# Kernel tuning notes

Measured on AMD Instinct MI355X. Metric: run time of the kernel, lower is better.

The kernel has to match this reference:

```python
import jax, jax.numpy as jnp
import numpy as np

N, E, B = 3000, 96000, 64
CIN, MID = 8, 16
G1, G2 = 32, 8
FC1, FC2, OUT = 512, 128, 10
EPS = 1e-5


def setup_inputs() -> dict:
    key = jax.random.key(0)
    ks = jax.random.split(key, 40)
    u = lambda k, shape, s: jax.random.uniform(k, shape, jnp.float32, -s, s)
    inp = {}
    inp['x'] = jax.random.normal(ks[0], (N, B, CIN), jnp.float32)
    inp['edge_index'] = jax.random.randint(ks[1], (2, E), 0, N, jnp.int64)
    # SAGEConv params (uniform(-1/sqrt(in_channels), ...))
    s = 1.0 / np.sqrt(CIN)
    inp['edge_w_raw'] = jnp.ones((E,), jnp.float32) * 0.01
    inp['sage_self_w'] = u(ks[2], (CIN, MID), s)
    inp['sage_w'] = u(ks[3], (CIN, MID), s)
    inp['sage_b'] = u(ks[4], (MID,), s)
    # LayerNorm over (num_nodes, mid_channel)
    inp['ln_g'] = jnp.ones((N, MID), jnp.float32)
    inp['ln_b'] = jnp.zeros((N, MID), jnp.float32)
    # 1x1 Conv2d stacks (stored as [out,in] matrices) + BatchNorm2d (eval stats)
    inp['conv1_w'] = jax.random.normal(ks[5], (G1, MID), jnp.float32) * np.sqrt(2.0 / G1)
    inp['conv1_b'] = u(ks[6], (G1,), 1.0 / np.sqrt(MID))
    inp['bn1_g'] = jax.random.uniform(ks[7], (G1,), jnp.float32, 0.5, 1.5)
    inp['bn1_b'] = jax.random.normal(ks[8], (G1,), jnp.float32) * 0.1
    inp['bn1_m'] = jax.random.normal(ks[9], (G1,), jnp.float32) * 0.1
    inp['bn1_v'] = jax.random.uniform(ks[10], (G1,), jnp.float32, 0.5, 1.5)
    inp['conv2_w'] = jax.random.normal(ks[11], (G2, G1), jnp.float32) * np.sqrt(2.0 / G2)
    inp['conv2_b'] = u(ks[12], (G2,), 1.0 / np.sqrt(G1))
    inp['bn2_g'] = jax.random.uniform(ks[13], (G2,), jnp.float32, 0.5, 1.5)
    inp['bn2_b'] = jax.random.normal(ks[14], (G2,), jnp.float32) * 0.1
    inp['bn2_m'] = jax.random.normal(ks[15], (G2,), jnp.float32) * 0.1
    inp['bn2_v'] = jax.random.uniform(ks[16], (G2,), jnp.float32, 0.5, 1.5)
    # FC stack: Linear(G2*N, FC1) + BN1d, Linear(FC1, FC2) + BN1d, fc1
    d0 = G2 * N
    inp['fc_w1'] = jax.random.normal(ks[17], (FC1, d0), jnp.float32) * np.sqrt(2.0 / (d0 + FC1))
    inp['fc_b1'] = jnp.full((FC1,), 0.01, jnp.float32)
    inp['bnf1_g'] = jax.random.uniform(ks[18], (FC1,), jnp.float32, 0.5, 1.5)
    inp['bnf1_b'] = jax.random.normal(ks[19], (FC1,), jnp.float32) * 0.1
    inp['bnf1_m'] = jax.random.normal(ks[20], (FC1,), jnp.float32) * 0.1
    inp['bnf1_v'] = jax.random.uniform(ks[21], (FC1,), jnp.float32, 0.5, 1.5)
    inp['fc_w2'] = jax.random.normal(ks[22], (FC2, FC1), jnp.float32) * np.sqrt(2.0 / (FC1 + FC2))
    inp['fc_b2'] = jnp.full((FC2,), 0.01, jnp.float32)
    inp['bnf2_g'] = jax.random.uniform(ks[23], (FC2,), jnp.float32, 0.5, 1.5)
    inp['bnf2_b'] = jax.random.normal(ks[24], (FC2,), jnp.float32) * 0.1
    inp['bnf2_m'] = jax.random.normal(ks[25], (FC2,), jnp.float32) * 0.1
    inp['bnf2_v'] = jax.random.uniform(ks[26], (FC2,), jnp.float32, 0.5, 1.5)
    inp['fc1_w'] = jax.random.normal(ks[27], (OUT, FC2), jnp.float32) * np.sqrt(2.0 / (FC2 + OUT))
    inp['fc1_b'] = jnp.full((OUT,), 0.01, jnp.float32)
    return inp


def _bn(y, g, b, m, v):
    # eval-mode BatchNorm; y is [B, C, N] or [B, C]
    if y.ndim == 3:
        return (y - m[:, None]) * (g[:, None] / jnp.sqrt(v[:, None] + EPS)) + b[:, None]
    return (y - m) * (g / jnp.sqrt(v + EPS)) + b


def reference(x, edge_index, edge_w_raw, sage_self_w, sage_w, sage_b, ln_g, ln_b,
              conv1_w, conv1_b, bn1_g, bn1_b, bn1_m, bn1_v,
              conv2_w, conv2_b, bn2_g, bn2_b, bn2_m, bn2_v,
              fc_w1, fc_b1, bnf1_g, bnf1_b, bnf1_m, bnf1_v,
              fc_w2, fc_b2, bnf2_g, bnf2_b, bnf2_m, bnf2_v,
              fc1_w, fc1_b):
    row, col = edge_index[0], edge_index[1]
    ew = jax.nn.sigmoid(edge_w_raw)
    # SAGEConv: gather -> weighted message -> scatter-mean by col -> matmul
    msg = x[row] * ew[:, None, None]                          # [E, B, CIN]
    summed = jax.ops.segment_sum(msg, col, num_segments=N)    # [N, B, CIN]
    cnt = jax.ops.segment_sum(jnp.ones((E,), x.dtype), col, num_segments=N)
    agg = summed / jnp.maximum(cnt, 1.0)[:, None, None]
    neigh = jnp.einsum('nbc,cm->nbm', agg, sage_w) + sage_b   # [N, B, MID]
    self_out = jnp.einsum('nbc,cm->nbm', x, sage_self_w)
    h = 0.0 * self_out + 1.0 * neigh                          # alphas = [0, 1]
    h = jax.nn.relu(h)
    # LayerNorm over (num_nodes, mid) per batch element
    hb = jnp.transpose(h, (1, 0, 2))                          # [B, N, MID]
    mu = hb.mean(axis=(1, 2), keepdims=True)
    var = hb.var(axis=(1, 2), keepdims=True)
    hb = (hb - mu) / jnp.sqrt(var + EPS) * ln_g + ln_b
    y = jnp.transpose(hb, (0, 2, 1))                          # [B, MID, N]
    # 1x1 conv stack (relu then BN, matching source order)
    y = jnp.einsum('om,bmn->bon', conv1_w, y) + conv1_b[:, None]
    y = _bn(jax.nn.relu(y), bn1_g, bn1_b, bn1_m, bn1_v)
    y = jnp.einsum('oc,bcn->bon', conv2_w, y) + conv2_b[:, None]
    y = _bn(jax.nn.relu(y), bn2_g, bn2_b, bn2_m, bn2_v)       # [B, G2, N]
    z = y.reshape(y.shape[0], -1)                             # [B, G2*N]
    z = jax.nn.relu(_bn(z @ fc_w1.T + fc_b1, bnf1_g, bnf1_b, bnf1_m, bnf1_v))
    z = jax.nn.relu(_bn(z @ fc_w2.T + fc_b2, bnf2_g, bnf2_b, bnf2_m, bnf2_v))
    logits = z @ fc1_w.T + fc1_b
    return jax.nn.softmax(logits, axis=-1), logits
```

## Files before the change

### kernel.cpp

```cpp
#include <hip/hip_runtime.h>
#include <hip/hip_bf16.h>
#include <math.h>

#define NN   3000
#define EE   96000
#define BB   64
#define CIN  8
#define MID  16
#define G1   32
#define G2   8
#define FC1N 512
#define FC2N 128
#define OUTN 10
#define EPSV 1e-5f

#define BC   (BB * CIN)
#define HROW (NN * MID)
#define D0   (G2 * NN)

#define P_EWRAW 0
#define P_SW    96000
#define P_SB    96128
#define P_LNG   96144
#define P_LNB   144144
#define P_C1W   192144
#define P_C1B   192656
#define P_BN1G  192688
#define P_BN1B  192720
#define P_BN1M  192752
#define P_BN1V  192784
#define P_C2W   192816
#define P_C2B   193072
#define P_BN2G  193080
#define P_BN2B  193088
#define P_BN2M  193096
#define P_BN2V  193104
#define P_FB1   193112
#define P_BF1G  193624
#define P_BF1B  194136
#define P_BF1M  194648
#define P_BF1V  195160
#define P_FW2   195672
#define P_FB2   261208
#define P_BF2G  261336
#define P_BF2B  261464
#define P_BF2M  261592
#define P_BF2V  261720
#define P_FOW   261848
#define P_FOB   263128
#define P_TOT   263138

#define KCH  320
#define NKC  75

__device__ __forceinline__ float b2f(unsigned short u) {
    union { unsigned int i; float f; } c;
    c.i = ((unsigned int)u) << 16;
    return c.f;
}

__device__ __forceinline__ unsigned short f2b_rne(float x) {
    union { float f; unsigned int u; } c; c.f = x;
    unsigned int r = c.u + 0x7FFFu + ((c.u >> 16) & 1u);
    return (unsigned short)(r >> 16);
}

typedef __attribute__((ext_vector_type(8))) short short8;
typedef __attribute__((ext_vector_type(4))) float f32x4;

struct PTab { const void* p[30]; };
__global__ __launch_bounds__(256)
void k_prep(const void* __restrict__ ei_raw, const unsigned int* __restrict__ ewr,
            PTab tab,
            int* __restrict__ ei32, int* __restrict__ cnt, int* __restrict__ flags,
            float* __restrict__ P) {
    __shared__ int sh_is64, sh_bf;
    if (threadIdx.x == 0) {
        const int* pw = (const int*)ei_raw;
        int any = 0;
        #pragma unroll
        for (int i = 1; i < 32; i += 2) any |= pw[i];
        sh_is64 = (any == 0) ? 1 : 0;
        unsigned int w = ewr[0];
        sh_bf = ((w >> 16) == (w & 0xFFFFu)) ? 1 : 0;
        if (blockIdx.x == 0) flags[0] = sh_bf;
    }
    __syncthreads();
    int bf = sh_bf;
    long long gi = (long long)blockIdx.x * blockDim.x + threadIdx.x;
    if (gi < 2 * EE) {
        int i = (int)gi;
        int v = sh_is64 ? (int)((const long long*)ei_raw)[i]
                        : ((const int*)ei_raw)[i];
        ei32[i] = v;
        if (i >= EE) atomicAdd(&cnt[v], 1);
        return;
    }
    gi -= 2 * EE;
    if (gi >= P_TOT) return;
    int i = (int)gi;
    const int off[31] = {
        P_EWRAW, P_SW, P_SB, P_LNG, P_LNB, P_C1W, P_C1B, P_BN1G, P_BN1B, P_BN1M,
        P_BN1V, P_C2W, P_C2B, P_BN2G, P_BN2B, P_BN2M, P_BN2V, P_FB1, P_BF1G,
        P_BF1B, P_BF1M, P_BF1V, P_FW2, P_FB2, P_BF2G, P_BF2B, P_BF2M, P_BF2V,
        P_FOW, P_FOB, P_TOT };
    int r = 0;
    #pragma unroll
    for (int j = 1; j < 31; ++j) r += (i >= off[j]) ? 1 : 0;
    int e = i - off[r];
    P[i] = bf ? b2f(((const unsigned short*)tab.p[r])[e])
              : ((const float*)tab.p[r])[e];
}

__global__ void k_scan(const int* __restrict__ cnt, int* __restrict__ off,
                       int* __restrict__ cursor) {
    __shared__ int part[1024];
    int t = threadIdx.x;
    int base = t * 3;
    int c0 = 0, c1 = 0, c2 = 0;
    if (base     < NN) c0 = cnt[base];
    if (base + 1 < NN) c1 = cnt[base + 1];
    if (base + 2 < NN) c2 = cnt[base + 2];
    int s = c0 + c1 + c2;
    part[t] = s;
    __syncthreads();
    for (int d = 1; d < 1024; d <<= 1) {
        int v = (t >= d) ? part[t - d] : 0;
        __syncthreads();
        part[t] += v;
        __syncthreads();
    }
    int excl = part[t] - s;
    if (base < NN)     { off[base]     = excl;           cursor[base]     = excl; }
    if (base + 1 < NN) { off[base + 1] = excl + c0;      cursor[base + 1] = excl + c0; }
    if (base + 2 < NN) { off[base + 2] = excl + c0 + c1; cursor[base + 2] = excl + c0 + c1; }
    if (t == 1023) off[NN] = part[1023];
}

__global__ void k_scatter(const int* __restrict__ ei, const float* __restrict__ ew,
                          int* __restrict__ cursor,
                          int* __restrict__ rcsr, float* __restrict__ wcsr) {
    int e = blockIdx.x * blockDim.x + threadIdx.x;
    if (e < EE) {
        int p = atomicAdd(&cursor[ei[EE + e]], 1);
        rcsr[p] = ei[e];
        wcsr[p] = 1.f / (1.f + expf(-ew[e]));
    }
}

__global__ __launch_bounds__(256)
void k_agg_sage(const void* __restrict__ xraw, const int* __restrict__ flags,
                const int* __restrict__ off,
                const int* __restrict__ rcsr, const float* __restrict__ wcsr,
                const float* __restrict__ sw, const float* __restrict__ sb,
                float* __restrict__ hb) {
    __shared__ float aggL[BC];
    __shared__ float swL[CIN * MID];
    __shared__ float sbL[MID];
    int n = blockIdx.x;
    int t = threadIdx.x;
    if (t < CIN * MID) swL[t] = sw[t];
    if (t < MID)       sbL[t] = sb[t];
    int k0 = off[n], k1 = off[n + 1];
    float a0 = 0.f, a1 = 0.f, b0 = 0.f, b1 = 0.f;
    int k = k0;
    if (flags[0]) {
        const unsigned int* xu = (const unsigned int*)xraw;
        for (; k + 3 < k1; k += 4) {
            int   r0 = rcsr[k],     r1 = rcsr[k + 1];
            int   r2 = rcsr[k + 2], r3 = rcsr[k + 3];
            float w0 = wcsr[k],     w1 = wcsr[k + 1];
            float w2 = wcsr[k + 2], w3 = wcsr[k + 3];
            unsigned int u0 = xu[(size_t)r0 * 256 + t];
            unsigned int u1 = xu[(size_t)r1 * 256 + t];
            unsigned int u2 = xu[(size_t)r2 * 256 + t];
            unsigned int u3 = xu[(size_t)r3 * 256 + t];
            a0 += b2f((unsigned short)(u0 & 0xFFFFu)) * w0;
            a1 += b2f((unsigned short)(u0 >> 16))     * w0;
            b0 += b2f((unsigned short)(u1 & 0xFFFFu)) * w1;
            b1 += b2f((unsigned short)(u1 >> 16))     * w1;
            a0 += b2f((unsigned short)(u2 & 0xFFFFu)) * w2;
            a1 += b2f((unsigned short)(u2 >> 16))     * w2;
            b0 += b2f((unsigned short)(u3 & 0xFFFFu)) * w3;
            b1 += b2f((unsigned short)(u3 >> 16))     * w3;
        }
        for (; k < k1; ++k) {
            int r0 = rcsr[k];
            float w0 = wcsr[k];
            unsigned int u0 = xu[(size_t)r0 * 256 + t];
            a0 += b2f((unsigned short)(u0 & 0xFFFFu)) * w0;
            a1 += b2f((unsigned short)(u0 >> 16))     * w0;
        }
        float inv = 1.f / fmaxf((float)(k1 - k0), 1.f);
        aggL[2 * t]     = (a0 + b0) * inv;
        aggL[2 * t + 1] = (a1 + b1) * inv;
    } else {
        const float* x = (const float*)xraw;
        for (; k + 3 < k1; k += 4) {
            int   r0 = rcsr[k],     r1 = rcsr[k + 1];
            int   r2 = rcsr[k + 2], r3 = rcsr[k + 3];
            float w0 = wcsr[k],     w1 = wcsr[k + 1];
            float w2 = wcsr[k + 2], w3 = wcsr[k + 3];
            const float* xp0 = x + (size_t)r0 * BC;
            const float* xp1 = x + (size_t)r1 * BC;
            const float* xp2 = x + (size_t)r2 * BC;
            const float* xp3 = x + (size_t)r3 * BC;
            a0 += xp0[t]       * w0;  a1 += xp0[t + 256] * w0;
            b0 += xp1[t]       * w1;  b1 += xp1[t + 256] * w1;
            a0 += xp2[t]       * w2;  a1 += xp2[t + 256] * w2;
            b0 += xp3[t]       * w3;  b1 += xp3[t + 256] * w3;
        }
        for (; k < k1; ++k) {
            int r0 = rcsr[k];
            float w0 = wcsr[k];
            const float* xp0 = x + (size_t)r0 * BC;
            a0 += xp0[t] * w0;
            a1 += xp0[t + 256] * w0;
        }
        float inv = 1.f / fmaxf((float)(k1 - k0), 1.f);
        aggL[t]       = (a0 + b0) * inv;
        aggL[t + 256] = (a1 + b1) * inv;
    }
    __syncthreads();
    #pragma unroll
    for (int r4 = 0; r4 < 4; ++r4) {
        int q = t + r4 * 256;
        int b = q >> 4, m = q & 15;
        float v = sbL[m];
        const float* ag = &aggL[b * CIN];
        #pragma unroll
        for (int c = 0; c < CIN; ++c) v += ag[c] * swL[c * MID + m];
        v = fmaxf(v, 0.f);
        hb[(size_t)b * HROW + n * MID + m] = v;
    }
}

__global__ __launch_bounds__(256)
void k_ln_stats(const float* __restrict__ hb, float* __restrict__ stats) {
    __shared__ float ssum[256], ssq[256];
    int b = blockIdx.x, t = threadIdx.x;
    const float4* p = (const float4*)(hb + (size_t)b * HROW);
    float s = 0.f, q = 0.f;
    for (int i = t; i < HROW / 4; i += 256) {
        float4 v = p[i];
        s += v.x + v.y + v.z + v.w;
        q += v.x * v.x + v.y * v.y + v.z * v.z + v.w * v.w;
    }
    ssum[t] = s; ssq[t] = q;
    __syncthreads();
    for (int d = 128; d > 0; d >>= 1) {
        if (t < d) { ssum[t] += ssum[t + d]; ssq[t] += ssq[t + d]; }
        __syncthreads();
    }
    if (t == 0) {
        float mu = ssum[0] / (float)HROW;
        float var = ssq[0] / (float)HROW - mu * mu;
        stats[b]      = mu;
        stats[BB + b] = 1.f / sqrtf(var + EPSV);
    }
}

__global__ __launch_bounds__(256)
void k_conv_stack(const float* __restrict__ hb, const float* __restrict__ stats,
                  const float* __restrict__ P, unsigned short* __restrict__ zT) {
    __shared__ float hbt[64 * 65];
    __shared__ float w1s[G1 * MID], w2s[G2 * G1];
    __shared__ float c1s[G1], s1[G1], t1[G1];
    __shared__ float c2s[G2], s2[G2], t2[G2];
    int t = threadIdx.x;
    int n0 = blockIdx.x * 4;
    for (int j = t; j < G1 * MID; j += 256) w1s[j] = P[P_C1W + j];
    if (t < G2 * G1)  w2s[t] = P[P_C2W + t];
    if (t < G1) {
        float s = P[P_BN1G + t] / sqrtf(P[P_BN1V + t] + EPSV);
        c1s[t] = P[P_C1B + t]; s1[t] = s; t1[t] = P[P_BN1B + t] - P[P_BN1M + t] * s;
    }
    if (t < G2) {
        float s = P[P_BN2G + t] / sqrtf(P[P_BN2V + t] + EPSV);
        c2s[t] = P[P_C2B + t]; s2[t] = s; t2[t] = P[P_BN2B + t] - P[P_BN2M + t] * s;
    }
    #pragma unroll
    for (int r = 0; r < 4; ++r) {
        int i = r * 256 + t;
        int b = i >> 4, q = i & 15;
        float4 v = *(const float4*)(hb + (size_t)b * HROW + n0 * MID + q * 4);
        int ld = b * 65 + q * 4;
        hbt[ld] = v.x; hbt[ld + 1] = v.y; hbt[ld + 2] = v.z; hbt[ld + 3] = v.w;
    }
    __syncthreads();
    int nl = t >> 6, b = t & 63;
    int n = n0 + nl;
    float mu = stats[b], rs = stats[BB + b];
    float tv[MID];
    #pragma unroll
    for (int m = 0; m < MID; ++m) {
        float g = P[P_LNG + n * MID + m], lb = P[P_LNB + n * MID + m];
        tv[m] = (hbt[b * 65 + nl * MID + m] - mu) * rs * g + lb;
    }
    float v1[G1];
    #pragma unroll
    for (int o = 0; o < G1; ++o) {
        float d = c1s[o];
        #pragma unroll
        for (int m = 0; m < MID; ++m) d += w1s[o * MID + m] * tv[m];
        d = fmaxf(d, 0.f);
        v1[o] = d * s1[o] + t1[o];
    }
    #pragma unroll
    for (int o2 = 0; o2 < G2; ++o2) {
        float d = c2s[o2];
        #pragma unroll
        for (int c = 0; c < G1; ++c) d += w2s[o2 * G1 + c] * v1[c];
        d = fmaxf(d, 0.f);
        zT[((size_t)(o2 * NN + n)) * BB + b] = f2b_rne(d * s2[o2] + t2[o2]);
    }
}

__global__ __launch_bounds__(256)
void k_fc1(const unsigned short* __restrict__ zT, const void* __restrict__ w1raw,
           const int* __restrict__ flags, float* __restrict__ out1p) {
    __shared__ unsigned int zs[64 * 20];
    int kc = blockIdx.y;
    int t = threadIdx.x;
    int lane = t & 63;
    int wv = t >> 6;
    int n = lane & 15;
    int q = lane >> 4;
    int fbase = blockIdx.x * 64 + wv * 16;
    int bf = flags[0];
    const size_t kcb = (size_t)kc * KCH;
    const float*          w1f = (const float*)w1raw;
    const unsigned short* w1b = (const unsigned short*)w1raw;

    f32x4 acc0 = {0.f, 0.f, 0.f, 0.f};
    f32x4 acc1 = {0.f, 0.f, 0.f, 0.f};
    f32x4 acc2 = {0.f, 0.f, 0.f, 0.f};
    f32x4 acc3 = {0.f, 0.f, 0.f, 0.f};

    int zb = t & 63;
    int kg = t >> 6;

    for (int ks = 0; ks < KCH / 32; ++ks) {
        size_t k0 = kcb + (size_t)ks * 32;
        const unsigned short* zsrc = zT + (k0 + kg * 8) * BB + zb;
        unsigned short zv[8];
        #pragma unroll
        for (int j = 0; j < 8; ++j) zv[j] = zsrc[j * BB];
        unsigned int pk0 = (unsigned int)zv[0] | ((unsigned int)zv[1] << 16);
        unsigned int pk1 = (unsigned int)zv[2] | ((unsigned int)zv[3] << 16);
        unsigned int pk2 = (unsigned int)zv[4] | ((unsigned int)zv[5] << 16);
        unsigned int pk3 = (unsigned int)zv[6] | ((unsigned int)zv[7] << 16);
        __syncthreads();
        *(uint4*)&zs[zb * 20 + kg * 4] = make_uint4(pk0, pk1, pk2, pk3);
        short8 av;
        if (bf) {
            av = *(const short8*)(w1b + (size_t)(fbase + n) * D0 + k0 + q * 8);
        } else {
            const float* wr = w1f + (size_t)(fbase + n) * D0 + k0 + q * 8;
            float4 wa = *(const float4*)wr;
            float4 wb = *(const float4*)(wr + 4);
            av[0] = (short)f2b_rne(wa.x); av[1] = (short)f2b_rne(wa.y);
            av[2] = (short)f2b_rne(wa.z); av[3] = (short)f2b_rne(wa.w);
            av[4] = (short)f2b_rne(wb.x); av[5] = (short)f2b_rne(wb.y);
            av[6] = (short)f2b_rne(wb.z); av[7] = (short)f2b_rne(wb.w);
        }
        __syncthreads();
        const char* zbase = (const char*)zs + q * 16;
        short8 bv0 = *(const short8*)(zbase + (0  + n) * 80);
        short8 bv1 = *(const short8*)(zbase + (16 + n) * 80);
        short8 bv2 = *(const short8*)(zbase + (32 + n) * 80);
        short8 bv3 = *(const short8*)(zbase + (48 + n) * 80);
        acc0 = __builtin_amdgcn_mfma_f32_16x16x32_bf16(av, bv0, acc0, 0, 0, 0);
        acc1 = __builtin_amdgcn_mfma_f32_16x16x32_bf16(av, bv1, acc1, 0, 0, 0);
        acc2 = __builtin_amdgcn_mfma_f32_16x16x32_bf16(av, bv2, acc2, 0, 0, 0);
        acc3 = __builtin_amdgcn_mfma_f32_16x16x32_bf16(av, bv3, acc3, 0, 0, 0);
    }
    float* op = out1p + ((size_t)kc * FC1N + fbase + q * 4) * BB + n;
    #pragma unroll
    for (int r = 0; r < 4; ++r) {
        op[r * BB +  0] = acc0[r];
        op[r * BB + 16] = acc1[r];
        op[r * BB + 32] = acc2[r];
        op[r * BB + 48] = acc3[r];
    }
}

__global__ void k_fc1_fin(const float* __restrict__ out1p, const float* __restrict__ P,
                          float* __restrict__ z1) {
    int i = blockIdx.x * blockDim.x + threadIdx.x;
    if (i < BB * FC1N) {
        int f = i >> 6, b = i & 63;
        float acc = 0.f;
        for (int kc = 0; kc < NKC; ++kc)
            acc += out1p[((size_t)kc * FC1N + f) * BB + b];
        acc += P[P_FB1 + f];
        float s = P[P_BF1G + f] / sqrtf(P[P_BF1V + f] + EPSV);
        acc = (acc - P[P_BF1M + f]) * s + P[P_BF1B + f];
        z1[b * FC1N + f] = fmaxf(acc, 0.f);
    }
}

__global__ __launch_bounds__(128)
void k_fc2head(const float* __restrict__ z1, const float* __restrict__ P,
               const int* __restrict__ flags, void* __restrict__ outv) {
    __shared__ float zsrc[FC1N];
    __shared__ float z2s[FC2N];
    __shared__ float lg[OUTN];
    __shared__ float red[2];
    int b = blockIdx.x, t = threadIdx.x;
    #pragma unroll
    for (int r = 0; r < 4; ++r) zsrc[t + r * 128] = z1[b * FC1N + t + r * 128];
    __syncthreads();
    {
        int f = t;
        const float4* wr = (const float4*)(P + P_FW2 + (size_t)f * FC1N);
        const float4* zr = (const float4*)zsrc;
        float acc = P[P_FB2 + f];
        for (int k = 0; k < FC1N / 4; ++k) {
            float4 wv = wr[k];
            float4 zv = zr[k];
            acc += wv.x * zv.x + wv.y * zv.y + wv.z * zv.z + wv.w * zv.w;
        }
        float s = P[P_BF2G + f] / sqrtf(P[P_BF2V + f] + EPSV);
        acc = (acc - P[P_BF2M + f]) * s + P[P_BF2B + f];
        z2s[f] = fmaxf(acc, 0.f);
    }
    __syncthreads();
    if (t < OUTN) {
        float acc = P[P_FOB + t];
        const float* wr = P + P_FOW + t * FC2N;
        for (int k = 0; k < FC2N; ++k) acc += wr[k] * z2s[k];
        lg[t] = acc;
    }
    __syncthreads();
    if (t == 0) {
        float mx = lg[0];
        for (int o = 1; o < OUTN; ++o) mx = fmaxf(mx, lg[o]);
        float s = 0.f;
        for (int o = 0; o < OUTN; ++o) s += expf(lg[o] - mx);
        red[0] = mx; red[1] = s;
    }
    __syncthreads();
    if (t < OUTN) {
        float p = expf(lg[t] - red[0]) / red[1];
        if (flags[0]) {
            __hip_bfloat16* o = (__hip_bfloat16*)outv;
            o[b * OUTN + t] = __float2bfloat16(p);
            o[BB * OUTN + b * OUTN + t] = __float2bfloat16(lg[t]);
        } else {
            float* o = (float*)outv;
            o[b * OUTN + t] = p;
            o[BB * OUTN + b * OUTN + t] = lg[t];
        }
    }
}

extern "C" void kernel_launch(void* const* d_in, const int* in_sizes, int n_in,
                              void* d_out, int out_size, void* d_ws, size_t ws_size,
                              hipStream_t stream) {
    char* ws = (char*)d_ws;
    size_t o = 0;
    auto carve = [&](size_t bytes) { void* p = ws + o; o += (bytes + 255) & ~(size_t)255; return p; };
    int*   flags  = (int*)  carve(16);
    int*   ei32   = (int*)  carve((size_t)2 * EE * sizeof(int));
    int*   cnt    = (int*)  carve(NN * sizeof(int));
    int*   off    = (int*)  carve((NN + 1) * sizeof(int));
    int*   cursor = (int*)  carve(NN * sizeof(int));
    int*   rcsr   = (int*)  carve(EE * sizeof(int));
    float* wcsr   = (float*)carve(EE * sizeof(float));
    float* P      = (float*)carve((size_t)P_TOT * sizeof(float));
    float* hb     = (float*)carve((size_t)BB * HROW * sizeof(float));
    float* stats  = (float*)carve(2 * BB * sizeof(float));
    unsigned short* zT = (unsigned short*)carve((size_t)D0 * BB * sizeof(unsigned short));
    float* out1p  = (float*)carve((size_t)NKC * FC1N * BB * sizeof(float));
    float* z1     = (float*)carve(BB * FC1N * sizeof(float));

    hipMemsetAsync(cnt, 0, NN * sizeof(int), stream);

    PTab tab;
    tab.p[0]  = d_in[2];   tab.p[1]  = d_in[4];   tab.p[2]  = d_in[5];
    tab.p[3]  = d_in[6];   tab.p[4]  = d_in[7];   tab.p[5]  = d_in[8];
    tab.p[6]  = d_in[9];   tab.p[7]  = d_in[10];  tab.p[8]  = d_in[11];
    tab.p[9]  = d_in[12];  tab.p[10] = d_in[13];  tab.p[11] = d_in[14];
    tab.p[12] = d_in[15];  tab.p[13] = d_in[16];  tab.p[14] = d_in[17];
    tab.p[15] = d_in[18];  tab.p[16] = d_in[19];  tab.p[17] = d_in[21];
    tab.p[18] = d_in[22];  tab.p[19] = d_in[23];  tab.p[20] = d_in[24];
    tab.p[21] = d_in[25];  tab.p[22] = d_in[26];  tab.p[23] = d_in[27];
    tab.p[24] = d_in[28];  tab.p[25] = d_in[29];  tab.p[26] = d_in[30];
    tab.p[27] = d_in[31];  tab.p[28] = d_in[32];  tab.p[29] = d_in[33];

    long long prep_tot = 2LL * EE + P_TOT;
    k_prep<<<(int)((prep_tot + 255) / 256), 256, 0, stream>>>(
        d_in[1], (const unsigned int*)d_in[2], tab, ei32, cnt, flags, P);

    k_scan   <<<1, 1024, 0, stream>>>(cnt, off, cursor);
    k_scatter<<<(EE + 255) / 256, 256, 0, stream>>>(ei32, P + P_EWRAW, cursor, rcsr, wcsr);
    k_agg_sage<<<NN, 256, 0, stream>>>(d_in[0], flags, off, rcsr, wcsr,
                                       P + P_SW, P + P_SB, hb);
    k_ln_stats<<<BB, 256, 0, stream>>>(hb, stats);
    k_conv_stack<<<NN / 4, 256, 0, stream>>>(hb, stats, P, zT);
    dim3 g7(FC1N / 64, NKC);
    k_fc1    <<<g7, 256, 0, stream>>>(zT, d_in[20], flags, out1p);
    k_fc1_fin<<<(BB * FC1N + 255) / 256, 256, 0, stream>>>(out1p, P, z1);
    k_fc2head<<<BB, 128, 0, stream>>>(z1, P, flags, (void*)d_out);
}
```

Before: 259.8 us.

## Fuse all stages into one persistent cooperative kernel with grid syncs

Replaces the chain of nine separate kernel launches plus a memset with a single cooperative persistent kernel. Stages are separated by grid-wide barriers, and each stage loops over its work with grid-stride indexing. LayerNorm statistics appear to be gathered during aggregation, and the FC1 K dimension is padded and rechunked to 64 chunks of 384. The aim is to remove launch gaps and extra passes. The costs are a grid capped at 512 blocks, occupancy limited to 2 blocks per SM, and serial phases such as the single-block scan that leave most of the GPU idle.

```diff
diff --git a/kernel.cpp b/kernel.cpp
--- a/kernel.cpp
+++ b/kernel.cpp
@@ -1,6 +1,9 @@
 #include <hip/hip_runtime.h>
 #include <hip/hip_bf16.h>
+#include <hip/hip_cooperative_groups.h>
 #include <math.h>
+
+namespace cg = cooperative_groups;
 
 #define NN   3000
 #define EE   96000
@@ -50,15 +53,15 @@
 #define P_FOB   263128
 #define P_TOT   263138
 
-#define KCH  320
-#define NKC  75
+#define KPAD 24576
+#define KCH  384
+#define NKC  64
 
 __device__ __forceinline__ float b2f(unsigned short u) {
     union { unsigned int i; float f; } c;
     c.i = ((unsigned int)u) << 16;
     return c.f;
 }
-
 __device__ __forceinline__ unsigned short f2b_rne(float x) {
     union { float f; unsigned int u; } c; c.f = x;
     unsigned int r = c.u + 0x7FFFu + ((c.u >> 16) & 1u);
@@ -69,388 +72,406 @@
 typedef __attribute__((ext_vector_type(4))) float f32x4;
 
 struct PTab { const void* p[30]; };
-__global__ __launch_bounds__(256)
-void k_prep(const void* __restrict__ ei_raw, const unsigned int* __restrict__ ewr,
-            PTab tab,
-            int* __restrict__ ei32, int* __restrict__ cnt, int* __restrict__ flags,
-            float* __restrict__ P) {
-    __shared__ int sh_is64, sh_bf;
-    if (threadIdx.x == 0) {
-        const int* pw = (const int*)ei_raw;
+
+struct MegaArgs {
+    const void* ei_raw;
+    const void* x_raw;
+    const void* w1raw;
+    PTab tab;
+    int* ei32; int* cnt; int* offA; int* cursor;
+    int* rcsr; float* wcsr; float* P;
+    float* hb; float* statsS; float* statsQ;
+    unsigned short* zT;
+    float* out1p; float* z1;
+    void* outv;
+};
+
+__global__ __launch_bounds__(256, 2)
+void k_mega(MegaArgs A) {
+    cg::grid_group grid = cg::this_grid();
+    __shared__ __align__(16) char smem[20768];
+    __shared__ int sh2[2];
+    const int t  = threadIdx.x;
+    const int nb = gridDim.x;
+    const int bid = blockIdx.x;
+
+    if (t == 0) {
+        const int* pw = (const int*)A.ei_raw;
         int any = 0;
         #pragma unroll
         for (int i = 1; i < 32; i += 2) any |= pw[i];
-        sh_is64 = (any == 0) ? 1 : 0;
-        unsigned int w = ewr[0];
-        sh_bf = ((w >> 16) == (w & 0xFFFFu)) ? 1 : 0;
-        if (blockIdx.x == 0) flags[0] = sh_bf;
+        sh2[0] = (any == 0) ? 1 : 0;
+        unsigned int w = ((const unsigned int*)A.tab.p[0])[0];
+        sh2[1] = ((w >> 16) == (w & 0xFFFFu)) ? 1 : 0;
     }
     __syncthreads();
-    int bf = sh_bf;
-    long long gi = (long long)blockIdx.x * blockDim.x + threadIdx.x;
-    if (gi < 2 * EE) {
-        int i = (int)gi;
-        int v = sh_is64 ? (int)((const long long*)ei_raw)[i]
-                        : ((const int*)ei_raw)[i];
-        ei32[i] = v;
-        if (i >= EE) atomicAdd(&cnt[v], 1);
-        return;
-    }
-    gi -= 2 * EE;
-    if (gi >= P_TOT) return;
-    int i = (int)gi;
-    const int off[31] = {
-        P_EWRAW, P_SW, P_SB, P_LNG, P_LNB, P_C1W, P_C1B, P_BN1G, P_BN1B, P_BN1M,
-        P_BN1V, P_C2W, P_C2B, P_BN2G, P_BN2B, P_BN2M, P_BN2V, P_FB1, P_BF1G,
-        P_BF1B, P_BF1M, P_BF1V, P_FW2, P_FB2, P_BF2G, P_BF2B, P_BF2M, P_BF2V,
-        P_FOW, P_FOB, P_TOT };
-    int r = 0;
-    #pragma unroll
-    for (int j = 1; j < 31; ++j) r += (i >= off[j]) ? 1 : 0;
-    int e = i - off[r];
-    P[i] = bf ? b2f(((const unsigned short*)tab.p[r])[e])
-              : ((const float*)tab.p[r])[e];
-}
-
-__global__ void k_scan(const int* __restrict__ cnt, int* __restrict__ off,
-                       int* __restrict__ cursor) {
-    __shared__ int part[1024];
-    int t = threadIdx.x;
-    int base = t * 3;
-    int c0 = 0, c1 = 0, c2 = 0;
-    if (base     < NN) c0 = cnt[base];
-    if (base + 1 < NN) c1 = cnt[base + 1];
-    if (base + 2 < NN) c2 = cnt[base + 2];
-    int s = c0 + c1 + c2;
-    part[t] = s;
-    __syncthreads();
-    for (int d = 1; d < 1024; d <<= 1) {
-        int v = (t >= d) ? part[t - d] : 0;
-        __syncthreads();
-        part[t] += v;
-        __syncthreads();
-    }
-    int excl = part[t] - s;
-    if (base < NN)     { off[base]     = excl;           cursor[base]     = excl; }
-    if (base + 1 < NN) { off[base + 1] = excl + c0;      cursor[base + 1] = excl + c0; }
-    if (base + 2 < NN) { off[base + 2] = excl + c0 + c1; cursor[base + 2] = excl + c0 + c1; }
-    if (t == 1023) off[NN] = part[1023];
-}
-
-__global__ void k_scatter(const int* __restrict__ ei, const float* __restrict__ ew,
-                          int* __restrict__ cursor,
-                          int* __restrict__ rcsr, float* __restrict__ wcsr) {
-    int e = blockIdx.x * blockDim.x + threadIdx.x;
-    if (e < EE) {
-        int p = atomicAdd(&cursor[ei[EE + e]], 1);
-        rcsr[p] = ei[e];
-        wcsr[p] = 1.f / (1.f + expf(-ew[e]));
-    }
-}
-
-__global__ __launch_bounds__(256)
-void k_agg_sage(const void* __restrict__ xraw, const int* __restrict__ flags,
-                const int* __restrict__ off,
-                const int* __restrict__ rcsr, const float* __restrict__ wcsr,
-                const float* __restrict__ sw, const float* __restrict__ sb,
-                float* __restrict__ hb) {
-    __shared__ float aggL[BC];
-    __shared__ float swL[CIN * MID];
-    __shared__ float sbL[MID];
-    int n = blockIdx.x;
-    int t = threadIdx.x;
-    if (t < CIN * MID) swL[t] = sw[t];
-    if (t < MID)       sbL[t] = sb[t];
-    int k0 = off[n], k1 = off[n + 1];
-    float a0 = 0.f, a1 = 0.f, b0 = 0.f, b1 = 0.f;
-    int k = k0;
-    if (flags[0]) {
-        const unsigned int* xu = (const unsigned int*)xraw;
-        for (; k + 3 < k1; k += 4) {
-            int   r0 = rcsr[k],     r1 = rcsr[k + 1];
-            int   r2 = rcsr[k + 2], r3 = rcsr[k + 3];
-            float w0 = wcsr[k],     w1 = wcsr[k + 1];
-            float w2 = wcsr[k + 2], w3 = wcsr[k + 3];
-            unsigned int u0 = xu[(size_t)r0 * 256 + t];
-            unsigned int u1 = xu[(size_t)r1 * 256 + t];
-            unsigned int u2 = xu[(size_t)r2 * 256 + t];
-            unsigned int u3 = xu[(size_t)r3 * 256 + t];
-            a0 += b2f((unsigned short)(u0 & 0xFFFFu)) * w0;
-            a1 += b2f((unsigned short)(u0 >> 16))     * w0;
-            b0 += b2f((unsigned short)(u1 & 0xFFFFu)) * w1;
-            b1 += b2f((unsigned short)(u1 >> 16))     * w1;
-            a0 += b2f((unsigned short)(u2 & 0xFFFFu)) * w2;
-            a1 += b2f((unsigned short)(u2 >> 16))     * w2;
-            b0 += b2f((unsigned short)(u3 & 0xFFFFu)) * w3;
-            b1 += b2f((unsigned short)(u3 >> 16))     * w3;
-        }
-        for (; k < k1; ++k) {
-            int r0 = rcsr[k];
-            float w0 = wcsr[k];
-            unsigned int u0 = xu[(size_t)r0 * 256 + t];
-            a0 += b2f((unsigned short)(u0 & 0xFFFFu)) * w0;
-            a1 += b2f((unsigned short)(u0 >> 16))     * w0;
-        }
-        float inv = 1.f / fmaxf((float)(k1 - k0), 1.f);
-        aggL[2 * t]     = (a0 + b0) * inv;
-        aggL[2 * t + 1] = (a1 + b1) * inv;
-    } else {
-        const float* x = (const float*)xraw;
-        for (; k + 3 < k1; k += 4) {
-            int   r0 = rcsr[k],     r1 = rcsr[k + 1];
-            int   r2 = rcsr[k + 2], r3 = rcsr[k + 3];
-            float w0 = wcsr[k],     w1 = wcsr[k + 1];
-            float w2 = wcsr[k + 2], w3 = wcsr[k + 3];
-            const float* xp0 = x + (size_t)r0 * BC;
-            const float* xp1 = x + (size_t)r1 * BC;
-            const float* xp2 = x + (size_t)r2 * BC;
-            const float* xp3 = x + (size_t)r3 * BC;
-            a0 += xp0[t]       * w0;  a1 += xp0[t + 256] * w0;
-            b0 += xp1[t]       * w1;  b1 += xp1[t + 256] * w1;
-            a0 += xp2[t]       * w2;  a1 += xp2[t + 256] * w2;
-            b0 += xp3[t]       * w3;  b1 += xp3[t + 256] * w3;
-        }
-        for (; k < k1; ++k) {
-            int r0 = rcsr[k];
-            float w0 = wcsr[k];
-            const float* xp0 = x + (size_t)r0 * BC;
-            a0 += xp0[t] * w0;
-            a1 += xp0[t + 256] * w0;
-        }
-        float inv = 1.f / fmaxf((float)(k1 - k0), 1.f);
-        aggL[t]       = (a0 + b0) * inv;
-        aggL[t + 256] = (a1 + b1) * inv;
-    }
-    __syncthreads();
-    #pragma unroll
-    for (int r4 = 0; r4 < 4; ++r4) {
-        int q = t + r4 * 256;
-        int b = q >> 4, m = q & 15;
-        float v = sbL[m];
-        const float* ag = &aggL[b * CIN];
+    const int is64 = sh2[0], bf = sh2[1];
+
+    for (int i = bid * 256 + t; i < NN; i += nb * 256) A.cnt[i] = 0;
+    for (int i = bid * 256 + t; i < BB; i += nb * 256) { A.statsS[i] = 0.f; A.statsQ[i] = 0.f; }
+    {
+        unsigned int* zp = (unsigned int*)(A.zT + (size_t)D0 * BB);
+        for (int i = bid * 256 + t; i < (KPAD - D0) * BB / 2; i += nb * 256) zp[i] = 0u;
+    }
+    grid.sync();
+    for (int i = bid * 256 + t; i < 2 * EE; i += nb * 256) {
+        int v = is64 ? (int)((const long long*)A.ei_raw)[i] : ((const int*)A.ei_raw)[i];
+        A.ei32[i] = v;
+        if (i >= EE) atomicAdd(&A.cnt[v], 1);
+    }
+    {
+        const int off[31] = {
+            P_EWRAW, P_SW, P_SB, P_LNG, P_LNB, P_C1W, P_C1B, P_BN1G, P_BN1B, P_BN1M,
+            P_BN1V, P_C2W, P_C2B, P_BN2G, P_BN2B, P_BN2M, P_BN2V, P_FB1, P_BF1G,
+            P_BF1B, P_BF1M, P_BF1V, P_FW2, P_FB2, P_BF2G, P_BF2B, P_BF2M, P_BF2V,
+            P_FOW, P_FOB, P_TOT };
+        for (int i = bid * 256 + t; i < P_TOT; i += nb * 256) {
+            int r = 0;
+            #pragma unroll
+            for (int j = 1; j < 31; ++j) r += (i >= off[j]) ? 1 : 0;
+            int e = i - off[r];
+            A.P[i] = bf ? b2f(((const unsigned short*)A.tab.p[r])[e])
+                        : ((const float*)A.tab.p[r])[e];
+        }
+    }
+    grid.sync();
+    if (bid == 0) {
+        int* tsum = (int*)smem;
+        int loc[12];
+        int base = t * 12;
+        int s = 0;
         #pragma unroll
-        for (int c = 0; c < CIN; ++c) v += ag[c] * swL[c * MID + m];
-        v = fmaxf(v, 0.f);
-        hb[(size_t)b * HROW + n * MID + m] = v;
-    }
-}
-
-__global__ __launch_bounds__(256)
-void k_ln_stats(const float* __restrict__ hb, float* __restrict__ stats) {
-    __shared__ float ssum[256], ssq[256];
-    int b = blockIdx.x, t = threadIdx.x;
-    const float4* p = (const float4*)(hb + (size_t)b * HROW);
-    float s = 0.f, q = 0.f;
-    for (int i = t; i < HROW / 4; i += 256) {
-        float4 v = p[i];
-        s += v.x + v.y + v.z + v.w;
-        q += v.x * v.x + v.y * v.y + v.z * v.z + v.w * v.w;
-    }
-    ssum[t] = s; ssq[t] = q;
-    __syncthreads();
-    for (int d = 128; d > 0; d >>= 1) {
-        if (t < d) { ssum[t] += ssum[t + d]; ssq[t] += ssq[t + d]; }
-        __syncthreads();
-    }
-    if (t == 0) {
-        float mu = ssum[0] / (float)HROW;
-        float var = ssq[0] / (float)HROW - mu * mu;
-        stats[b]      = mu;
-        stats[BB + b] = 1.f / sqrtf(var + EPSV);
-    }
-}
-
-__global__ __launch_bounds__(256)
-void k_conv_stack(const float* __restrict__ hb, const float* __restrict__ stats,
-                  const float* __restrict__ P, unsigned short* __restrict__ zT) {
-    __shared__ float hbt[64 * 65];
-    __shared__ float w1s[G1 * MID], w2s[G2 * G1];
-    __shared__ float c1s[G1], s1[G1], t1[G1];
-    __shared__ float c2s[G2], s2[G2], t2[G2];
-    int t = threadIdx.x;
-    int n0 = blockIdx.x * 4;
-    for (int j = t; j < G1 * MID; j += 256) w1s[j] = P[P_C1W + j];
-    if (t < G2 * G1)  w2s[t] = P[P_C2W + t];
-    if (t < G1) {
-        float s = P[P_BN1G + t] / sqrtf(P[P_BN1V + t] + EPSV);
-        c1s[t] = P[P_C1B + t]; s1[t] = s; t1[t] = P[P_BN1B + t] - P[P_BN1M + t] * s;
-    }
-    if (t < G2) {
-        float s = P[P_BN2G + t] / sqrtf(P[P_BN2V + t] + EPSV);
-        c2s[t] = P[P_C2B + t]; s2[t] = s; t2[t] = P[P_BN2B + t] - P[P_BN2M + t] * s;
-    }
-    #pragma unroll
-    for (int r = 0; r < 4; ++r) {
-        int i = r * 256 + t;
-        int b = i >> 4, q = i & 15;
-        float4 v = *(const float4*)(hb + (size_t)b * HROW + n0 * MID + q * 4);
-        int ld = b * 65 + q * 4;
-        hbt[ld] = v.x; hbt[ld + 1] = v.y; hbt[ld + 2] = v.z; hbt[ld + 3] = v.w;
-    }
-    __syncthreads();
-    int nl = t >> 6, b = t & 63;
-    int n = n0 + nl;
-    float mu = stats[b], rs = stats[BB + b];
-    float tv[MID];
-    #pragma unroll
-    for (int m = 0; m < MID; ++m) {
-        float g = P[P_LNG + n * MID + m], lb = P[P_LNB + n * MID + m];
-        tv[m] = (hbt[b * 65 + nl * MID + m] - mu) * rs * g + lb;
-    }
-    float v1[G1];
-    #pragma unroll
-    for (int o = 0; o < G1; ++o) {
-        float d = c1s[o];
+        for (int j = 0; j < 12; ++j) {
+            int c = (base + j < NN) ? A.cnt[base + j] : 0;
+            loc[j] = s; s += c;
+        }
+        tsum[t] = s;
+        __syncthreads();
+        for (int d = 1; d < 256; d <<= 1) {
+            int v = (t >= d) ? tsum[t - d] : 0;
+            __syncthreads();
+            tsum[t] += v;
+            __syncthreads();
+        }
+        int excl = tsum[t] - s;
         #pragma unroll
-        for (int m = 0; m < MID; ++m) d += w1s[o * MID + m] * tv[m];
-        d = fmaxf(d, 0.f);
-        v1[o] = d * s1[o] + t1[o];
-    }
-    #pragma unroll
-    for (int o2 = 0; o2 < G2; ++o2) {
-        float d = c2s[o2];
+        for (int j = 0; j < 12; ++j) {
+            if (base + j < NN) {
+                int o = excl + loc[j];
+                A.offA[base + j] = o;
+                A.cursor[base + j] = o;
+            }
+        }
+        if (t == 255) A.offA[NN] = tsum[255];
+    }
+    grid.sync();
+    for (int e = bid * 256 + t; e < EE; e += nb * 256) {
+        int p = atomicAdd(&A.cursor[A.ei32[EE + e]], 1);
+        A.rcsr[p] = A.ei32[e];
+        A.wcsr[p] = 1.f / (1.f + expf(-A.P[P_EWRAW + e]));
+    }
+    grid.sync();
+    {
+        float* aggL = (float*)smem;
+        float* swL  = aggL + BC;
+        float* sbL  = swL + CIN * MID;
+        float* lnS  = sbL + MID;
+        float* lnQ  = lnS + BB;
+        if (t < CIN * MID) swL[t] = A.P[P_SW + t];
+        if (t < MID)       sbL[t] = A.P[P_SB + t];
+        if (t < BB) { lnS[t] = 0.f; lnQ[t] = 0.f; }
+        float accS[4] = {0.f, 0.f, 0.f, 0.f};
+        float accQ[4] = {0.f, 0.f, 0.f, 0.f};
+        __syncthreads();
+        for (int n = bid; n < NN; n += nb) {
+            int k0 = A.offA[n], k1 = A.offA[n + 1];
+            float a0 = 0.f, a1 = 0.f, b0 = 0.f, b1 = 0.f;
+            int k = k0;
+            if (bf) {
+                const unsigned int* xu = (const unsigned int*)A.x_raw;
+                for (; k + 3 < k1; k += 4) {
+                    int   r0 = A.rcsr[k],     r1 = A.rcsr[k + 1];
+                    int   r2 = A.rcsr[k + 2], r3 = A.rcsr[k + 3];
+                    float w0 = A.wcsr[k],     w1 = A.wcsr[k + 1];
+                    float w2 = A.wcsr[k + 2], w3 = A.wcsr[k + 3];
+                    unsigned int u0 = xu[(size_t)r0 * 256 + t];
+                    unsigned int u1 = xu[(size_t)r1 * 256 + t];
+                    unsigned int u2 = xu[(size_t)r2 * 256 + t];
+                    unsigned int u3 = xu[(size_t)r3 * 256 + t];
+                    a0 += b2f((unsigned short)(u0 & 0xFFFFu)) * w0;
+                    a1 += b2f((unsigned short)(u0 >> 16))     * w0;
+                    b0 += b2f((unsigned short)(u1 & 0xFFFFu)) * w1;
+                    b1 += b2f((unsigned short)(u1 >> 16))     * w1;
+                    a0 += b2f((unsigned short)(u2 & 0xFFFFu)) * w2;
+                    a1 += b2f((unsigned short)(u2 >> 16))     * w2;
+                    b0 += b2f((unsigned short)(u3 & 0xFFFFu)) * w3;
+                    b1 += b2f((unsigned short)(u3 >> 16))     * w3;
+                }
+                for (; k < k1; ++k) {
+                    int r0 = A.rcsr[k];
+                    float w0 = A.wcsr[k];
+                    unsigned int u0 = xu[(size_t)r0 * 256 + t];
+                    a0 += b2f((unsigned short)(u0 & 0xFFFFu)) * w0;
+                    a1 += b2f((unsigned short)(u0 >> 16))     * w0;
+                }
+            } else {
+                const float* x = (const float*)A.x_raw;
+                for (; k + 3 < k1; k += 4) {
+                    int   r0 = A.rcsr[k],     r1 = A.rcsr[k + 1];
+                    int   r2 = A.rcsr[k + 2], r3 = A.rcsr[k + 3];
+                    float w0 = A.wcsr[k],     w1 = A.wcsr[k + 1];
+                    float w2 = A.wcsr[k + 2], w3 = A.wcsr[k + 3];
+                    const float* xp0 = x + (size_t)r0 * BC;
+                    const float* xp1 = x + (size_t)r1 * BC;
+                    const float* xp2 = x + (size_t)r2 * BC;
+                    const float* xp3 = x + (size_t)r3 * BC;
+                    a0 += xp0[t] * w0;  a1 += xp0[t + 256] * w0;
+                    b0 += xp1[t] * w1;  b1 += xp1[t + 256] * w1;
+                    a0 += xp2[t] * w2;  a1 += xp2[t + 256] * w2;
+                    b0 += xp3[t] * w3;  b1 += xp3[t + 256] * w3;
+                }
+                for (; k < k1; ++k) {
+                    int r0 = A.rcsr[k];
+                    float w0 = A.wcsr[k];
+                    const float* xp0 = x + (size_t)r0 * BC;
+                    a0 += xp0[t] * w0;
+                    a1 += xp0[t + 256] * w0;
+                }
+            }
+            float inv = 1.f / fmaxf((float)(k1 - k0), 1.f);
+            __syncthreads();
+            if (bf) {
+                aggL[2 * t]     = (a0 + b0) * inv;
+                aggL[2 * t + 1] = (a1 + b1) * inv;
+            } else {
+                aggL[t]       = (a0 + b0) * inv;
+                aggL[t + 256] = (a1 + b1) * inv;
+            }
+            __syncthreads();
+            #pragma unroll
+            for (int r4 = 0; r4 < 4; ++r4) {
+                int q = t + r4 * 256;
+                int b = q >> 4, m = q & 15;
+                float v = sbL[m];
+                const float* ag = &aggL[b * CIN];
+                #pragma unroll
+                for (int c = 0; c < CIN; ++c) v += ag[c] * swL[c * MID + m];
+                v = fmaxf(v, 0.f);
+                A.hb[(size_t)b * HROW + n * MID + m] = v;
+                accS[r4] += v;
+                accQ[r4] += v * v;
+            }
+        }
+        __syncthreads();
         #pragma unroll
-        for (int c = 0; c < G1; ++c) d += w2s[o2 * G1 + c] * v1[c];
-        d = fmaxf(d, 0.f);
-        zT[((size_t)(o2 * NN + n)) * BB + b] = f2b_rne(d * s2[o2] + t2[o2]);
-    }
-}
-
-__global__ __launch_bounds__(256)
-void k_fc1(const unsigned short* __restrict__ zT, const void* __restrict__ w1raw,
-           const int* __restrict__ flags, float* __restrict__ out1p) {
-    __shared__ unsigned int zs[64 * 20];
-    int kc = blockIdx.y;
-    int t = threadIdx.x;
-    int lane = t & 63;
-    int wv = t >> 6;
-    int n = lane & 15;
-    int q = lane >> 4;
-    int fbase = blockIdx.x * 64 + wv * 16;
-    int bf = flags[0];
-    const size_t kcb = (size_t)kc * KCH;
-    const float*          w1f = (const float*)w1raw;
-    const unsigned short* w1b = (const unsigned short*)w1raw;
-
-    f32x4 acc0 = {0.f, 0.f, 0.f, 0.f};
-    f32x4 acc1 = {0.f, 0.f, 0.f, 0.f};
-    f32x4 acc2 = {0.f, 0.f, 0.f, 0.f};
-    f32x4 acc3 = {0.f, 0.f, 0.f, 0.f};
-
-    int zb = t & 63;
-    int kg = t >> 6;
-
-    for (int ks = 0; ks < KCH / 32; ++ks) {
-        size_t k0 = kcb + (size_t)ks * 32;
-        const unsigned short* zsrc = zT + (k0 + kg * 8) * BB + zb;
-        unsigned short zv[8];
-        #pragma unroll
-        for (int j = 0; j < 8; ++j) zv[j] = zsrc[j * BB];
-        unsigned int pk0 = (unsigned int)zv[0] | ((unsigned int)zv[1] << 16);
-        unsigned int pk1 = (unsigned int)zv[2] | ((unsigned int)zv[3] << 16);
-        unsigned int pk2 = (unsigned int)zv[4] | ((unsigned int)zv[5] << 16);
-        unsigned int pk3 = (unsigned int)zv[6] | ((unsigned int)zv[7] << 16);
-        __syncthreads();
-        *(uint4*)&zs[zb * 20 + kg * 4] = make_uint4(pk0, pk1, pk2, pk3);
-        short8 av;
-        if (bf) {
-            av = *(const short8*)(w1b + (size_t)(fbase + n) * D0 + k0 + q * 8);
-        } else {
-            const float* wr = w1f + (size_t)(fbase + n) * D0 + k0 + q * 8;
-            float4 wa = *(const float4*)wr;
-            float4 wb = *(const float4*)(wr + 4);
-            av[0] = (short)f2b_rne(wa.x); av[1] = (short)f2b_rne(wa.y);
-            av[2] = (short)f2b_rne(wa.z); av[3] = (short)f2b_rne(wa.w);
-            av[4] = (short)f2b_rne(wb.x); av[5] = (short)f2b_rne(wb.y);
-            av[6] = (short)f2b_rne(wb.z); av[7] = (short)f2b_rne(wb.w);
-        }
-        __syncthreads();
-        const char* zbase = (const char*)zs + q * 16;
-        short8 bv0 = *(const short8*)(zbase + (0  + n) * 80);
-        short8 bv1 = *(const short8*)(zbase + (16 + n) * 80);
-        short8 bv2 = *(const short8*)(zbase + (32 + n) * 80);
-        short8 bv3 = *(const short8*)(zbase + (48 + n) * 80);
-        acc0 = __builtin_amdgcn_mfma_f32_16x16x32_bf16(av, bv0, acc0, 0, 0, 0);
-        acc1 = __builtin_amdgcn_mfma_f32_16x16x32_bf16(av, bv1, acc1, 0, 0, 0);
-        acc2 = __builtin_amdgcn_mfma_f32_16x16x32_bf16(av, bv2, acc2, 0, 0, 0);
-        acc3 = __builtin_amdgcn_mfma_f32_16x16x32_bf16(av, bv3, acc3, 0, 0, 0);
-    }
-    float* op = out1p + ((size_t)kc * FC1N + fbase + q * 4) * BB + n;
-    #pragma unroll
-    for (int r = 0; r < 4; ++r) {
-        op[r * BB +  0] = acc0[r];
-        op[r * BB + 16] = acc1[r];
-        op[r * BB + 32] = acc2[r];
-        op[r * BB + 48] = acc3[r];
-    }
-}
-
-__global__ void k_fc1_fin(const float* __restrict__ out1p, const float* __restrict__ P,
-                          float* __restrict__ z1) {
-    int i = blockIdx.x * blockDim.x + threadIdx.x;
-    if (i < BB * FC1N) {
+        for (int r4 = 0; r4 < 4; ++r4) {
+            int b = (t + r4 * 256) >> 4;
+            atomicAdd(&lnS[b], accS[r4]);
+            atomicAdd(&lnQ[b], accQ[r4]);
+        }
+        __syncthreads();
+        if (t < BB) {
+            atomicAdd(&A.statsS[t], lnS[t]);
+            atomicAdd(&A.statsQ[t], lnQ[t]);
+        }
+    }
+    grid.sync();
+    {
+        float* hbt = (float*)smem;
+        float* w1s = hbt + 64 * 65;
+        float* w2s = w1s + G1 * MID;
+        float* c1s = w2s + G2 * G1;
+        float* s1  = c1s + G1;
+        float* t1  = s1 + G1;
+        float* c2s = t1 + G1;
+        float* s2  = c2s + G2;
+        float* t2  = s2 + G2;
+        float* muL = t2 + G2;
+        float* rsL = muL + BB;
+        for (int j = t; j < G1 * MID; j += 256) w1s[j] = A.P[P_C1W + j];
+        if (t < G2 * G1) w2s[t] = A.P[P_C2W + t];
+        if (t < G1) {
+            float s = A.P[P_BN1G + t] / sqrtf(A.P[P_BN1V + t] + EPSV);
+            c1s[t] = A.P[P_C1B + t]; s1[t] = s; t1[t] = A.P[P_BN1B + t] - A.P[P_BN1M + t] * s;
+        }
+        if (t < G2) {
+            float s = A.P[P_BN2G + t] / sqrtf(A.P[P_BN2V + t] + EPSV);
+            c2s[t] = A.P[P_C2B + t]; s2[t] = s; t2[t] = A.P[P_BN2B + t] - A.P[P_BN2M + t] * s;
+        }
+        if (t < BB) {
+            float mu = A.statsS[t] / (float)HROW;
+            float var = A.statsQ[t] / (float)HROW - mu * mu;
+            muL[t] = mu;
+            rsL[t] = 1.f / sqrtf(var + EPSV);
+        }
+        for (int vb = bid; vb < NN / 4; vb += nb) {
+            int n0 = vb * 4;
+            __syncthreads();
+            #pragma unroll
+            for (int r = 0; r < 4; ++r) {
+                int i = r * 256 + t;
+                int b = i >> 4, q = i & 15;
+                float4 v = *(const float4*)(A.hb + (size_t)b * HROW + n0 * MID + q * 4);
+                int ld = b * 65 + q * 4;
+                hbt[ld] = v.x; hbt[ld + 1] = v.y; hbt[ld + 2] = v.z; hbt[ld + 3] = v.w;
+            }
+            __syncthreads();
+            int nl = t >> 6, b = t & 63;
+            int n = n0 + nl;
+            float mu = muL[b], rs = rsL[b];
+            float tv[MID];
+            #pragma unroll
+            for (int m = 0; m < MID; ++m) {
+                float g = A.P[P_LNG + n * MID + m], lb = A.P[P_LNB + n * MID + m];
+                tv[m] = (hbt[b * 65 + nl * MID + m] - mu) * rs * g + lb;
+            }
+            float v1[G1];
+            #pragma unroll
+            for (int o = 0; o < G1; ++o) {
+                float d = c1s[o];
+                #pragma unroll
+                for (int m = 0; m < MID; ++m) d += w1s[o * MID + m] * tv[m];
+                d = fmaxf(d, 0.f);
+                v1[o] = d * s1[o] + t1[o];
+            }
+            #pragma unroll
+            for (int o2 = 0; o2 < G2; ++o2) {
+                float d = c2s[o2];
+                #pragma unroll
+                for (int c = 0; c < G1; ++c) d += w2s[o2 * G1 + c] * v1[c];
+                d = fmaxf(d, 0.f);
+                A.zT[((size_t)(o2 * NN + n)) * BB + b] = f2b_rne(d * s2[o2] + t2[o2]);
+            }
+        }
+    }
+    grid.sync();
+    {
+        unsigned int* zs = (unsigned int*)smem;
+        const float*          w1f = (const float*)A.w1raw;
+        const unsigned short* w1b = (const unsigned short*)A.w1raw;
+        int lane = t & 63;
+        int wv = t >> 6;
+        int n = lane & 15;
+        int q = lane >> 4;
+        int zb = t & 63;
+        int kg = t >> 6;
+        for (int vb = bid; vb < 8 * NKC; vb += nb) {
+            int fg = vb & 7, kc = vb >> 3;
+            int fbase = fg * 64 + wv * 16;
+            const size_t kcb = (size_t)kc * KCH;
+            f32x4 acc0 = {0.f, 0.f, 0.f, 0.f};
+            f32x4 acc1 = {0.f, 0.f, 0.f, 0.f};
+            f32x4 acc2 = {0.f, 0.f, 0.f, 0.f};
+            f32x4 acc3 = {0.f, 0.f, 0.f, 0.f};
+            for (int ks = 0; ks < KCH / 32; ++ks) {
+                size_t k0 = kcb + (size_t)ks * 32;
+                const unsigned short* zsrc = A.zT + (k0 + kg * 8) * BB + zb;
+                unsigned short zv[8];
+                #pragma unroll
+                for (int j = 0; j < 8; ++j) zv[j] = zsrc[j * BB];
+                unsigned int pk0 = (unsigned int)zv[0] | ((unsigned int)zv[1] << 16);
+                unsigned int pk1 = (unsigned int)zv[2] | ((unsigned int)zv[3] << 16);
+                unsigned int pk2 = (unsigned int)zv[4] | ((unsigned int)zv[5] << 16);
+                unsigned int pk3 = (unsigned int)zv[6] | ((unsigned int)zv[7] << 16);
+                __syncthreads();
+                *(uint4*)&zs[zb * 20 + kg * 4] = make_uint4(pk0, pk1, pk2, pk3);
+                short8 av = {0, 0, 0, 0, 0, 0, 0, 0};
+                if (k0 < D0) {
+                    if (bf) {
+                        av = *(const short8*)(w1b + (size_t)(fbase + n) * D0 + k0 + q * 8);
+                    } else {
+                        const float* wr = w1f + (size_t)(fbase + n) * D0 + k0 + q * 8;
+                        float4 wa = *(const float4*)wr;
+                        float4 wb = *(const float4*)(wr + 4);
+                        av[0] = (short)f2b_rne(wa.x); av[1] = (short)f2b_rne(wa.y);
+                        av[2] = (short)f2b_rne(wa.z); av[3] = (short)f2b_rne(wa.w);
+                        av[4] = (short)f2b_rne(wb.x); av[5] = (short)f2b_rne(wb.y);
+                        av[6] = (short)f2b_rne(wb.z); av[7] = (short)f2b_rne(wb.w);
+                    }
+                }
+                __syncthreads();
+                const char* zbase = (const char*)zs + q * 16;
+                short8 bv0 = *(const short8*)(zbase + (0  + n) * 80);
+                short8 bv1 = *(const short8*)(zbase + (16 + n) * 80);
+                short8 bv2 = *(const short8*)(zbase + (32 + n) * 80);
+                short8 bv3 = *(const short8*)(zbase + (48 + n) * 80);
+                acc0 = __builtin_amdgcn_mfma_f32_16x16x32_bf16(av, bv0, acc0, 0, 0, 0);
+                acc1 = __builtin_amdgcn_mfma_f32_16x16x32_bf16(av, bv1, acc1, 0, 0, 0);
+                acc2 = __builtin_amdgcn_mfma_f32_16x16x32_bf16(av, bv2, acc2, 0, 0, 0);
+                acc3 = __builtin_amdgcn_mfma_f32_16x16x32_bf16(av, bv3, acc3, 0, 0, 0);
+            }
+            float* op = A.out1p + ((size_t)kc * FC1N + fbase + q * 4) * BB + n;
+            #pragma unroll
+            for (int r = 0; r < 4; ++r) {
+                op[r * BB +  0] = acc0[r];
+                op[r * BB + 16] = acc1[r];
+                op[r * BB + 32] = acc2[r];
+                op[r * BB + 48] = acc3[r];
+            }
+        }
+    }
+    grid.sync();
+    for (int i = bid * 256 + t; i < BB * FC1N; i += nb * 256) {
         int f = i >> 6, b = i & 63;
         float acc = 0.f;
         for (int kc = 0; kc < NKC; ++kc)
-            acc += out1p[((size_t)kc * FC1N + f) * BB + b];
-        acc += P[P_FB1 + f];
-        float s = P[P_BF1G + f] / sqrtf(P[P_BF1V + f] + EPSV);
-        acc = (acc - P[P_BF1M + f]) * s + P[P_BF1B + f];
-        z1[b * FC1N + f] = fmaxf(acc, 0.f);
-    }
-}
-
-__global__ __launch_bounds__(128)
-void k_fc2head(const float* __restrict__ z1, const float* __restrict__ P,
-               const int* __restrict__ flags, void* __restrict__ outv) {
-    __shared__ float zsrc[FC1N];
-    __shared__ float z2s[FC2N];
-    __shared__ float lg[OUTN];
-    __shared__ float red[2];
-    int b = blockIdx.x, t = threadIdx.x;
-    #pragma unroll
-    for (int r = 0; r < 4; ++r) zsrc[t + r * 128] = z1[b * FC1N + t + r * 128];
-    __syncthreads();
-    {
-        int f = t;
-        const float4* wr = (const float4*)(P + P_FW2 + (size_t)f * FC1N);
-        const float4* zr = (const float4*)zsrc;
-        float acc = P[P_FB2 + f];
-        for (int k = 0; k < FC1N / 4; ++k) {
-            float4 wv = wr[k];
-            float4 zv = zr[k];
-            acc += wv.x * zv.x + wv.y * zv.y + wv.z * zv.z + wv.w * zv.w;
-        }
-        float s = P[P_BF2G + f] / sqrtf(P[P_BF2V + f] + EPSV);
-        acc = (acc - P[P_BF2M + f]) * s + P[P_BF2B + f];
-        z2s[f] = fmaxf(acc, 0.f);
-    }
-    __syncthreads();
-    if (t < OUTN) {
-        float acc = P[P_FOB + t];
-        const float* wr = P + P_FOW + t * FC2N;
-        for (int k = 0; k < FC2N; ++k) acc += wr[k] * z2s[k];
-        lg[t] = acc;
-    }
-    __syncthreads();
-    if (t == 0) {
-        float mx = lg[0];
-        for (int o = 1; o < OUTN; ++o) mx = fmaxf(mx, lg[o]);
-        float s = 0.f;
-        for (int o = 0; o < OUTN; ++o) s += expf(lg[o] - mx);
-        red[0] = mx; red[1] = s;
-    }
-    __syncthreads();
-    if (t < OUTN) {
-        float p = expf(lg[t] - red[0]) / red[1];
-        if (flags[0]) {
-            __hip_bfloat16* o = (__hip_bfloat16*)outv;
-            o[b * OUTN + t] = __float2bfloat16(p);
-            o[BB * OUTN + b * OUTN + t] = __float2bfloat16(lg[t]);
-        } else {
-            float* o = (float*)outv;
-            o[b * OUTN + t] = p;
-            o[BB * OUTN + b * OUTN + t] = lg[t];
+            acc += A.out1p[((size_t)kc * FC1N + f) * BB + b];
+        acc += A.P[P_FB1 + f];
+        float s = A.P[P_BF1G + f] / sqrtf(A.P[P_BF1V + f] + EPSV);
+        acc = (acc - A.P[P_BF1M + f]) * s + A.P[P_BF1B + f];
+        A.z1[b * FC1N + f] = fmaxf(acc, 0.f);
+    }
+    grid.sync();
+    if (bid < BB) {
+        float* zsrc = (float*)smem;
+        float* z2s  = zsrc + FC1N;
+        float* lg   = z2s + FC2N;
+        float* red  = lg + 12;
+        int b = bid;
+        zsrc[t]       = A.z1[b * FC1N + t];
+        zsrc[t + 256] = A.z1[b * FC1N + t + 256];
+        __syncthreads();
+        if (t < FC2N) {
+            int f = t;
+            const float4* wr = (const float4*)(A.P + P_FW2 + (size_t)f * FC1N);
+            const float4* zr = (const float4*)zsrc;
+            float acc = A.P[P_FB2 + f];
+            for (int k = 0; k < FC1N / 4; ++k) {
+                float4 wv = wr[k];
+                float4 zv = zr[k];
+                acc += wv.x * zv.x + wv.y * zv.y + wv.z * zv.z + wv.w * zv.w;
+            }
+            float s = A.P[P_BF2G + f] / sqrtf(A.P[P_BF2V + f] + EPSV);
+            acc = (acc - A.P[P_BF2M + f]) * s + A.P[P_BF2B + f];
+            z2s[f] = fmaxf(acc, 0.f);
+        }
+        __syncthreads();
+        if (t < OUTN) {
+            float acc = A.P[P_FOB + t];
+            const float* wr = A.P + P_FOW + t * FC2N;
+            for (int k = 0; k < FC2N; ++k) acc += wr[k] * z2s[k];
+            lg[t] = acc;
+        }
+        __syncthreads();
+        if (t == 0) {
+            float mx = lg[0];
+            for (int o = 1; o < OUTN; ++o) mx = fmaxf(mx, lg[o]);
+            float s = 0.f;
+            for (int o = 0; o < OUTN; ++o) s += expf(lg[o] - mx);
+            red[0] = mx; red[1] = s;
+        }
+        __syncthreads();
+        if (t < OUTN) {
+            float p = expf(lg[t] - red[0]) / red[1];
+            if (bf) {
+                __hip_bfloat16* o = (__hip_bfloat16*)A.outv;
+                o[b * OUTN + t] = __float2bfloat16(p);
+                o[BB * OUTN + b * OUTN + t] = __float2bfloat16(lg[t]);
+            } else {
+                float* o = (float*)A.outv;
+                o[b * OUTN + t] = p;
+                o[BB * OUTN + b * OUTN + t] = lg[t];
+            }
         }
     }
 }
@@ -461,46 +482,42 @@
     char* ws = (char*)d_ws;
     size_t o = 0;
     auto carve = [&](size_t bytes) { void* p = ws + o; o += (bytes + 255) & ~(size_t)255; return p; };
-    int*   flags  = (int*)  carve(16);
-    int*   ei32   = (int*)  carve((size_t)2 * EE * sizeof(int));
-    int*   cnt    = (int*)  carve(NN * sizeof(int));
-    int*   off    = (int*)  carve((NN + 1) * sizeof(int));
-    int*   cursor = (int*)  carve(NN * sizeof(int));
-    int*   rcsr   = (int*)  carve(EE * sizeof(int));
-    float* wcsr   = (float*)carve(EE * sizeof(float));
-    float* P      = (float*)carve((size_t)P_TOT * sizeof(float));
-    float* hb     = (float*)carve((size_t)BB * HROW * sizeof(float));
-    float* stats  = (float*)carve(2 * BB * sizeof(float));
-    unsigned short* zT = (unsigned short*)carve((size_t)D0 * BB * sizeof(unsigned short));
-    float* out1p  = (float*)carve((size_t)NKC * FC1N * BB * sizeof(float));
-    float* z1     = (float*)carve(BB * FC1N * sizeof(float));
-
-    hipMemsetAsync(cnt, 0, NN * sizeof(int), stream);
-
-    PTab tab;
-    tab.p[0]  = d_in[2];   tab.p[1]  = d_in[4];   tab.p[2]  = d_in[5];
-    tab.p[3]  = d_in[6];   tab.p[4]  = d_in[7];   tab.p[5]  = d_in[8];
-    tab.p[6]  = d_in[9];   tab.p[7]  = d_in[10];  tab.p[8]  = d_in[11];
-    tab.p[9]  = d_in[12];  tab.p[10] = d_in[13];  tab.p[11] = d_in[14];
-    tab.p[12] = d_in[15];  tab.p[13] = d_in[16];  tab.p[14] = d_in[17];
-    tab.p[15] = d_in[18];  tab.p[16] = d_in[19];  tab.p[17] = d_in[21];
-    tab.p[18] = d_in[22];  tab.p[19] = d_in[23];  tab.p[20] = d_in[24];
-    tab.p[21] = d_in[25];  tab.p[22] = d_in[26];  tab.p[23] = d_in[27];
-    tab.p[24] = d_in[28];  tab.p[25] = d_in[29];  tab.p[26] = d_in[30];
-    tab.p[27] = d_in[31];  tab.p[28] = d_in[32];  tab.p[29] = d_in[33];
-
-    long long prep_tot = 2LL * EE + P_TOT;
-    k_prep<<<(int)((prep_tot + 255) / 256), 256, 0, stream>>>(
-        d_in[1], (const unsigned int*)d_in[2], tab, ei32, cnt, flags, P);
-
-    k_scan   <<<1, 1024, 0, stream>>>(cnt, off, cursor);
-    k_scatter<<<(EE + 255) / 256, 256, 0, stream>>>(ei32, P + P_EWRAW, cursor, rcsr, wcsr);
-    k_agg_sage<<<NN, 256, 0, stream>>>(d_in[0], flags, off, rcsr, wcsr,
-                                       P + P_SW, P + P_SB, hb);
-    k_ln_stats<<<BB, 256, 0, stream>>>(hb, stats);
-    k_conv_stack<<<NN / 4, 256, 0, stream>>>(hb, stats, P, zT);
-    dim3 g7(FC1N / 64, NKC);
-    k_fc1    <<<g7, 256, 0, stream>>>(zT, d_in[20], flags, out1p);
-    k_fc1_fin<<<(BB * FC1N + 255) / 256, 256, 0, stream>>>(out1p, P, z1);
-    k_fc2head<<<BB, 128, 0, stream>>>(z1, P, flags, (void*)d_out);
+    MegaArgs A;
+    A.ei32   = (int*)  carve((size_t)2 * EE * sizeof(int));
+    A.cnt    = (int*)  carve(NN * sizeof(int));
+    A.offA   = (int*)  carve((NN + 1) * sizeof(int));
+    A.cursor = (int*)  carve(NN * sizeof(int));
+    A.rcsr   = (int*)  carve(EE * sizeof(int));
+    A.wcsr   = (float*)carve(EE * sizeof(float));
+    A.P      = (float*)carve((size_t)P_TOT * sizeof(float));
+    A.hb     = (float*)carve((size_t)BB * HROW * sizeof(float));
+    A.statsS = (float*)carve(BB * sizeof(float));
+    A.statsQ = (float*)carve(BB * sizeof(float));
+    A.zT     = (unsigned short*)carve((size_t)KPAD * BB * sizeof(unsigned short));
+    A.out1p  = (float*)carve((size_t)NKC * FC1N * BB * sizeof(float));
+    A.z1     = (float*)carve(BB * FC1N * sizeof(float));
+
+    A.ei_raw = d_in[1];
+    A.x_raw  = d_in[0];
+    A.w1raw  = d_in[20];
+    A.outv   = d_out;
+    A.tab.p[0]  = d_in[2];   A.tab.p[1]  = d_in[4];   A.tab.p[2]  = d_in[5];
+    A.tab.p[3]  = d_in[6];   A.tab.p[4]  = d_in[7];   A.tab.p[5]  = d_in[8];
+    A.tab.p[6]  = d_in[9];   A.tab.p[7]  = d_in[10];  A.tab.p[8]  = d_in[11];
+    A.tab.p[9]  = d_in[12];  A.tab.p[10] = d_in[13];  A.tab.p[11] = d_in[14];
+    A.tab.p[12] = d_in[15];  A.tab.p[13] = d_in[16];  A.tab.p[14] = d_in[17];
+    A.tab.p[15] = d_in[18];  A.tab.p[16] = d_in[19];  A.tab.p[17] = d_in[21];
+    A.tab.p[18] = d_in[22];  A.tab.p[19] = d_in[23];  A.tab.p[20] = d_in[24];
+    A.tab.p[21] = d_in[25];  A.tab.p[22] = d_in[26];  A.tab.p[23] = d_in[27];
+    A.tab.p[24] = d_in[28];  A.tab.p[25] = d_in[29];  A.tab.p[26] = d_in[30];
+    A.tab.p[27] = d_in[31];  A.tab.p[28] = d_in[32];  A.tab.p[29] = d_in[33];
+
+    int maxB = 0;
+    if (hipOccupancyMaxActiveBlocksPerMultiprocessor(&maxB, k_mega, 256, 0) != hipSuccess
+        || maxB < 1) maxB = 1;
+    int grid = maxB * 256;
+    if (grid > 512) grid = 512;
+
+    void* args[] = { (void*)&A };
+    hipLaunchCooperativeKernel((void*)k_mega, dim3(grid), dim3(256), args, 0, stream);
 }
```

New measurement: 727.2 us. 2.8x slower.
